# Performance work log

Hardware: AMD Instinct MI355X
Metric: run time of the kernel (lower is better)

Reference implementation:

```python
import jax, jax.numpy as jnp
import numpy as np

N, F_IN, F_HID, F_OUT, E = 100000, 128, 256, 40, 1600000
LOG_SQRT_2PI = 0.9189385332046727  # log(sqrt(2*pi))


def setup_inputs() -> dict:
    key = jax.random.key(0)
    ks = jax.random.split(key, 12)
    s_in = 1.0 / np.sqrt(F_IN)
    s_hid = 1.0 / np.sqrt(F_HID)
    s_out = 1.0 / np.sqrt(F_OUT)
    return {
        "x": jax.random.normal(ks[0], (N, F_IN), jnp.float32),
        "adj_row": jax.random.randint(ks[1], (E,), 0, N, jnp.int32),
        "adj_col": jax.random.randint(ks[2], (E,), 0, N, jnp.int32),
        "adj_val": jax.random.uniform(ks[3], (E,), jnp.float32) * 0.1,
        "eps": jax.random.normal(ks[4], (1, N, F_IN), jnp.float32),
        "Wz1": jax.random.normal(ks[5], (F_IN, F_IN), jnp.float32) * s_in,
        "bz1": jnp.zeros((F_IN,), jnp.float32),
        "Wz2": jax.random.normal(ks[6], (F_IN, 2 * F_IN), jnp.float32) * s_in,
        "bz2": jnp.zeros((2 * F_IN,), jnp.float32),
        "W0": jax.random.uniform(ks[7], (F_IN, F_HID), jnp.float32, -s_hid, s_hid),
        "b0": jax.random.uniform(ks[8], (F_HID,), jnp.float32, -s_hid, s_hid),
        "W1": jax.random.uniform(ks[9], (F_HID, F_OUT), jnp.float32, -s_out, s_out),
        "b1": jax.random.uniform(ks[10], (F_OUT,), jnp.float32, -s_out, s_out),
    }


def spmm(row, col, val, mat):
    # sparse [N,N] (COO) @ dense [N,D] -> [N,D] via gather + segment_sum
    return jax.ops.segment_sum(val[:, None] * mat[col], row, num_segments=mat.shape[0])


def reference(x, adj_row, adj_col, adj_val, eps, Wz1, bz1, Wz2, bz2, W0, b0, W1, b1):
    # z_w MLP: Linear -> ReLU -> Linear producing [N, 2*F_IN]
    feats = jax.nn.relu(x @ Wz1 + bz1) @ Wz2 + bz2
    z_x_hat = spmm(adj_row, adj_col, adj_val, feats)  # [N, 2*F_IN]
    mean = z_x_hat[:, :F_IN]
    std = jax.nn.softplus(z_x_hat[:, F_IN:]) + 0.01
    # rsample((1,)): [1, N, F_IN]
    z = mean[None] + std[None] * eps
    # diagonal Normal log-probs, summed over feature dim
    logq = (-0.5 * ((z - mean[None]) / std[None]) ** 2 - jnp.log(std)[None] - LOG_SQRT_2PI).sum(-1)
    logp = (-0.5 * z ** 2 - LOG_SQRT_2PI).sum(-1)
    l2 = (logq - logp).mean(0).mean()
    h = z.mean(0)  # [N, F_IN]
    # GCN layer 1: dense transform then spmm, relu (dropout off in eval)
    h = jax.nn.relu(spmm(adj_row, adj_col, adj_val, h @ W0) + b0)
    # GCN layer 2 (output)
    out = spmm(adj_row, adj_col, adj_val, h @ W1) + b1
    return jax.nn.log_softmax(out, axis=1), l2
```

## Files before the change

### kernel.cpp

```cpp
#include <hip/hip_runtime.h>
#include <math.h>

constexpr int NN = 100000;
constexpr int NCHUNK = 128;
constexpr int RROWS  = 12500;

using f32x4 = __attribute__((ext_vector_type(4))) float;
using s16x8 = __attribute__((ext_vector_type(8))) short;
using us8   = __attribute__((ext_vector_type(8))) unsigned short;
using us4   = __attribute__((ext_vector_type(4))) unsigned short;

__device__ __forceinline__ unsigned short f2bf(float f) {
    unsigned u = __float_as_uint(f);
    unsigned r = u + 0x7FFFu + ((u >> 16) & 1u);
    return (unsigned short)(r >> 16);
}
__device__ __forceinline__ float bf2f(unsigned short u) {
    return __uint_as_float(((unsigned)u) << 16);
}

__device__ __forceinline__ void wfrag_body(
    const float* __restrict__ W, short* __restrict__ Wf,
    int K, int NC, int tid)
{
    const int KK = K / 32;
    int lane = tid & 63, f = tid >> 6;
    int ncg = f / KK, kk = f % KK;
    int col = ncg * 16 + (lane & 15);
    int k0  = kk * 32 + 8 * (lane >> 4);
    s16x8 o;
    #pragma unroll
    for (int j = 0; j < 8; ++j)
        o[j] = (col < NC) ? (short)f2bf(W[(size_t)(k0 + j) * NC + col]) : (short)0;
    *reinterpret_cast<s16x8*>(Wf + (size_t)tid * 8) = o;
}

template<int K, int WM, int WN, int CB, int AK, bool OBF16, int BIASMODE, bool ORELU>
__device__ __forceinline__ void gemm_body(
    int bid, const void* __restrict__ Ain, const short* __restrict__ Wf,
    const float* __restrict__ bias, const float* __restrict__ b0,
    void* __restrict__ Cout, int M, int NCout)
{
    constexpr int KK = K / 32;
    const int tid = threadIdx.x;
    const int lane = tid & 63, wid = tid >> 6;
    const int wm = wid % WM, wn = wid / WM;
    const int rowBase = bid * (WM * 64) + wm * 64;
    const int cfb = wn * CB;
    const int l15 = lane & 15, lh = lane >> 4;

    f32x4 acc[4][CB];
    #pragma unroll
    for (int i = 0; i < 4; ++i)
        #pragma unroll
        for (int j = 0; j < CB; ++j) acc[i][j] = (f32x4)0.f;

    #pragma unroll
    for (int kk = 0; kk < KK; ++kk) {
        const int k0 = kk * 32 + lh * 8;
        s16x8 a[4];
        #pragma unroll
        for (int rb = 0; rb < 4; ++rb) {
            int row = rowBase + rb * 16 + l15;
            row = row < M ? row : M - 1;
            if (AK == 0) {
                const float* ap = (const float*)Ain + (size_t)row * K + k0;
                float4 u = *reinterpret_cast<const float4*>(ap);
                float4 v = *reinterpret_cast<const float4*>(ap + 4);
                a[rb][0] = (short)f2bf(u.x); a[rb][1] = (short)f2bf(u.y);
                a[rb][2] = (short)f2bf(u.z); a[rb][3] = (short)f2bf(u.w);
                a[rb][4] = (short)f2bf(v.x); a[rb][5] = (short)f2bf(v.y);
                a[rb][6] = (short)f2bf(v.z); a[rb][7] = (short)f2bf(v.w);
            } else if (AK == 1) {
                a[rb] = *reinterpret_cast<const s16x8*>((const short*)Ain + (size_t)row * K + k0);
            } else {
                s16x8 s = *reinterpret_cast<const s16x8*>((const short*)Ain + (size_t)row * K + k0);
                float4 ba = *reinterpret_cast<const float4*>(b0 + k0);
                float4 bb = *reinterpret_cast<const float4*>(b0 + k0 + 4);
                float bv[8] = {ba.x, ba.y, ba.z, ba.w, bb.x, bb.y, bb.z, bb.w};
                #pragma unroll
                for (int j = 0; j < 8; ++j) {
                    float fv = bf2f((unsigned short)s[j]) + bv[j];
                    a[rb][j] = (short)f2bf(fmaxf(fv, 0.f));
                }
            }
        }
        s16x8 b[CB];
        #pragma unroll
        for (int cb = 0; cb < CB; ++cb)
            b[cb] = *reinterpret_cast<const s16x8*>(
                Wf + ((size_t)((cfb + cb) * KK + kk) * 64 + lane) * 8);
        #pragma unroll
        for (int rb = 0; rb < 4; ++rb)
            #pragma unroll
            for (int cb = 0; cb < CB; ++cb)
                acc[rb][cb] = __builtin_amdgcn_mfma_f32_16x16x32_bf16(
                    a[rb], b[cb], acc[rb][cb], 0, 0, 0);
    }

    #pragma unroll
    for (int cb = 0; cb < CB; ++cb) {
        int col = (cfb + cb) * 16 + l15;
        if (col >= NCout) continue;
        float bs = (BIASMODE != 0) ? bias[col] : 0.f;
        #pragma unroll
        for (int rb = 0; rb < 4; ++rb) {
            #pragma unroll
            for (int r = 0; r < 4; ++r) {
                int row = rowBase + rb * 16 + lh * 4 + r;
                if (row >= M) continue;
                float v = acc[rb][cb][r];
                if (BIASMODE == 1) v += bs;
                if (ORELU) v = fmaxf(v, 0.f);
                if (OBF16)
                    ((unsigned short*)Cout)[(size_t)row * NCout + col] = f2bf(v);
                else
                    ((float*)Cout)[(size_t)row * NCout + col] = v;
            }
        }
    }
}

template<int K, int WM, int WN, int CB, int AK, bool OBF16, int BIASMODE, bool ORELU>
__global__ __launch_bounds__(WM * WN * 64) void gemm_mfma(
    const void* __restrict__ Ain, const short* __restrict__ Wf,
    const float* __restrict__ bias, const float* __restrict__ b0,
    void* __restrict__ Cout, int M, int NCout)
{
    gemm_body<K, WM, WN, CB, AK, OBF16, BIASMODE, ORELU>(
        blockIdx.x, Ain, Wf, bias, b0, Cout, M, NCout);
}

__device__ __forceinline__ void hist_body(
    const int* __restrict__ row, unsigned short* __restrict__ part,
    int E, int chunkE, int chunk, int rowLo, unsigned* lcnt)
{
    for (int i = threadIdx.x; i < RROWS / 4; i += 256) lcnt[i] = 0u;
    __syncthreads();
    const int e0 = chunk * chunkE;
    const int e1 = min(e0 + chunkE, E);
    for (int e = e0 + threadIdx.x; e < e1; e += 256) {
        int lr = row[e] - rowLo;
        if ((unsigned)lr < (unsigned)RROWS)
            atomicAdd(&lcnt[lr >> 2], 1u << ((lr & 3) << 3));
    }
    __syncthreads();
    unsigned* dst = reinterpret_cast<unsigned*>(part + (size_t)chunk * NN + rowLo);
    for (int i = threadIdx.x; i < RROWS / 4; i += 256) {
        unsigned w = lcnt[i];
        dst[2 * i + 0] = (w & 0xFFu) | (((w >> 8) & 0xFFu) << 16);
        dst[2 * i + 1] = ((w >> 16) & 0xFFu) | (((w >> 24) & 0xFFu) << 16);
    }
}

__device__ __forceinline__ void scatter_body(
    const int* __restrict__ row, const int* __restrict__ col,
    const float* __restrict__ val, const int* __restrict__ rp,
    const unsigned short* __restrict__ part, int2* __restrict__ edges,
    int E, int chunkE, int chunk, int rowLo, unsigned* lcnt)
{
    for (int i = threadIdx.x; i < RROWS / 4; i += 256) lcnt[i] = 0u;
    __syncthreads();
    const int e0 = chunk * chunkE;
    const int e1 = min(e0 + chunkE, E);
    const unsigned short* choff = part + (size_t)chunk * NN;
    for (int e = e0 + threadIdx.x; e < e1; e += 256) {
        int r = row[e];
        int lr = r - rowLo;
        if ((unsigned)lr < (unsigned)RROWS) {
            unsigned old = atomicAdd(&lcnt[lr >> 2], 1u << ((lr & 3) << 3));
            int local = (int)((old >> ((lr & 3) << 3)) & 0xFFu);
            int p = rp[r] + (int)choff[r] + local;
            edges[p] = make_int2(col[e], __float_as_int(val[e]));
        }
    }
}

__global__ __launch_bounds__(256) void hist_wfrag_combo(
    const int* __restrict__ arow, unsigned short* __restrict__ part,
    int E, int chunkE,
    const float* __restrict__ Wz1, const float* __restrict__ Wz2,
    const float* __restrict__ W0,  const float* __restrict__ W1,
    short* wz1f, short* wz2f, short* w0f, short* w1f)
{
    __shared__ unsigned lcnt[RROWS / 4];
    int b = blockIdx.x;
    if (b < NCHUNK * 8) {
        hist_body(arow, part, E, chunkE, b & (NCHUNK - 1), (b >> 7) * RROWS, lcnt);
    } else {
        int bb = b - NCHUNK * 8;
        if (bb < 8)       wfrag_body(Wz1, wz1f, 128, 128, bb * 256 + threadIdx.x);
        else if (bb < 24) wfrag_body(Wz2, wz2f, 128, 256, (bb - 8) * 256 + threadIdx.x);
        else if (bb < 40) wfrag_body(W0,  w0f,  128, 256, (bb - 24) * 256 + threadIdx.x);
        else {
            int tid = (bb - 40) * 256 + threadIdx.x;
            if (tid < 3 * 8 * 64) wfrag_body(W1, w1f, 256, 40, tid);
        }
    }
}

__global__ __launch_bounds__(256) void scatter_g1_combo(
    const int* __restrict__ arow, const int* __restrict__ acol,
    const float* __restrict__ aval, const int* __restrict__ rp,
    const unsigned short* __restrict__ part, int2* __restrict__ edges,
    int E, int chunkE,
    const float* __restrict__ x, const short* __restrict__ wz1f,
    const float* __restrict__ bz1, unsigned short* __restrict__ t1out)
{
    __shared__ unsigned lcnt[RROWS / 4];
    int b = blockIdx.x;
    if (b < NCHUNK * 8) {
        scatter_body(arow, acol, aval, rp, part, edges, E, chunkE,
                     b & (NCHUNK - 1), (b >> 7) * RROWS, lcnt);
    } else {
        gemm_body<128, 2, 2, 4, 0, true, 1, true>(
            b - NCHUNK * 8, x, wz1f, bz1, nullptr, t1out, NN, 128);
    }
}

__global__ __launch_bounds__(256) void chunk_scan(
    unsigned short* __restrict__ part, int* __restrict__ cnt)
{
    int r = blockIdx.x * 256 + threadIdx.x;
    if (r >= NN) return;
    int run = 0;
    for (int c0 = 0; c0 < NCHUNK; c0 += 8) {
        int v[8];
        #pragma unroll
        for (int j = 0; j < 8; ++j) v[j] = part[(size_t)(c0 + j) * NN + r];
        #pragma unroll
        for (int j = 0; j < 8; ++j) {
            part[(size_t)(c0 + j) * NN + r] = (unsigned short)run;
            run += v[j];
        }
    }
    cnt[r] = run;
}

__global__ __launch_bounds__(256) void scan_blk(
    const int* __restrict__ cnt, int* __restrict__ rp, int* __restrict__ bsums, int n)
{
    const int t = threadIdx.x;
    const int lane = t & 63, wid = t >> 6;
    const int base = blockIdx.x * 1024 + t * 4;
    int a0 = 0, a1 = 0, a2 = 0, a3 = 0;
    if (base + 3 < n) {
        int4 v = *reinterpret_cast<const int4*>(&cnt[base]);
        a0 = v.x; a1 = v.y; a2 = v.z; a3 = v.w;
    } else {
        if (base + 0 < n) a0 = cnt[base + 0];
        if (base + 1 < n) a1 = cnt[base + 1];
        if (base + 2 < n) a2 = cnt[base + 2];
        if (base + 3 < n) a3 = cnt[base + 3];
    }
    int s0 = a0, s1 = s0 + a1, s2 = s1 + a2, s3 = s2 + a3;
    int v = s3;
    #pragma unroll
    for (int o = 1; o < 64; o <<= 1) {
        int u = __shfl_up(v, o);
        if (lane >= o) v += u;
    }
    __shared__ int wtot[4];
    if (lane == 63) wtot[wid] = v;
    __syncthreads();
    int woff = 0;
    #pragma unroll
    for (int w = 0; w < 4; ++w) if (w < wid) woff += wtot[w];
    int texcl = woff + v - s3;
    if (base + 0 < n) rp[base + 0] = texcl;
    if (base + 1 < n) rp[base + 1] = texcl + s0;
    if (base + 2 < n) rp[base + 2] = texcl + s1;
    if (base + 3 < n) rp[base + 3] = texcl + s2;
    if (t == 255) bsums[blockIdx.x] = woff + v;
}

__global__ void scan_mid(const int* __restrict__ bsums, int* __restrict__ boff, int nb)
{
    if (threadIdx.x == 0 && blockIdx.x == 0) {
        int run = 0;
        for (int b = 0; b < nb; ++b) { boff[b] = run; run += bsums[b]; }
    }
}

__global__ __launch_bounds__(256) void scan_add(
    int* __restrict__ rp, const int* __restrict__ boff, int n, int E)
{
    int i = blockIdx.x * 256 + threadIdx.x;
    if (i < n) rp[i] += boff[i >> 10];
    if (i == 0) rp[n] = E;
}

template<bool RS>
__global__ __launch_bounds__(256) void spmm128(
    const int* __restrict__ rp, const int2* __restrict__ edges,
    const unsigned short* __restrict__ mat, unsigned short* __restrict__ out,
    float* __restrict__ rowsum)
{
    int gid = blockIdx.x * 256 + threadIdx.x;
    int r = gid >> 4, sl = gid & 15;
    if (r >= NN) return;
    const int beg = rp[r], end = rp[r + 1];
    float acc[8] = {};
    float vs = 0.f;
    int e = beg;
    for (; e + 7 < end; e += 8) {
        int2 c[8]; float v[8]; us8 f[8];
        #pragma unroll
        for (int k = 0; k < 8; ++k) c[k] = edges[e + k];
        #pragma unroll
        for (int k = 0; k < 8; ++k) {
            v[k] = __int_as_float(c[k].y);
            f[k] = *reinterpret_cast<const us8*>(mat + (size_t)c[k].x * 128 + sl * 8);
        }
        if (RS) vs += v[0] + v[1] + v[2] + v[3] + v[4] + v[5] + v[6] + v[7];
        #pragma unroll
        for (int k = 0; k < 8; ++k)
            #pragma unroll
            for (int j = 0; j < 8; ++j) acc[j] += v[k] * bf2f(f[k][j]);
    }
    for (; e + 3 < end; e += 4) {
        int2 c[4]; float v[4]; us8 f[4];
        #pragma unroll
        for (int k = 0; k < 4; ++k) c[k] = edges[e + k];
        #pragma unroll
        for (int k = 0; k < 4; ++k) {
            v[k] = __int_as_float(c[k].y);
            f[k] = *reinterpret_cast<const us8*>(mat + (size_t)c[k].x * 128 + sl * 8);
        }
        if (RS) vs += v[0] + v[1] + v[2] + v[3];
        #pragma unroll
        for (int k = 0; k < 4; ++k)
            #pragma unroll
            for (int j = 0; j < 8; ++j) acc[j] += v[k] * bf2f(f[k][j]);
    }
    for (; e < end; ++e) {
        int2 cv = edges[e];
        float v = __int_as_float(cv.y);
        if (RS) vs += v;
        us8 f = *reinterpret_cast<const us8*>(mat + (size_t)cv.x * 128 + sl * 8);
        #pragma unroll
        for (int j = 0; j < 8; ++j) acc[j] += v * bf2f(f[j]);
    }
    us8 o;
    #pragma unroll
    for (int j = 0; j < 8; ++j) o[j] = f2bf(acc[j]);
    *reinterpret_cast<us8*>(out + (size_t)r * 128 + sl * 8) = o;
    if (RS && sl == 0) rowsum[r] = vs;
}

__global__ __launch_bounds__(256) void gemm_z_sample(
    const unsigned short* __restrict__ A, const short* __restrict__ Wf,
    const float* __restrict__ bz2, const float* __restrict__ rowsum,
    const float* __restrict__ eps, unsigned short* __restrict__ hout,
    float* __restrict__ partials)
{
    const int tid = threadIdx.x;
    const int lane = tid & 63, wid = tid >> 6;
    const int rowBase = blockIdx.x * 64;
    const int l15 = lane & 15, lh = lane >> 4;

    const int cf[4] = {wid * 2, wid * 2 + 1, 8 + wid * 2, 8 + wid * 2 + 1};

    f32x4 acc[4][4];
    #pragma unroll
    for (int i = 0; i < 4; ++i)
        #pragma unroll
        for (int j = 0; j < 4; ++j) acc[i][j] = (f32x4)0.f;

    #pragma unroll
    for (int kk = 0; kk < 4; ++kk) {
        const int k0 = kk * 32 + lh * 8;
        s16x8 a[4];
        #pragma unroll
        for (int rb = 0; rb < 4; ++rb) {
            int row = rowBase + rb * 16 + l15;
            row = row < NN ? row : NN - 1;
            a[rb] = *reinterpret_cast<const s16x8*>(A + (size_t)row * 128 + k0);
        }
        s16x8 b[4];
        #pragma unroll
        for (int cb = 0; cb < 4; ++cb)
            b[cb] = *reinterpret_cast<const s16x8*>(
                Wf + ((size_t)(cf[cb] * 4 + kk) * 64 + lane) * 8);
        #pragma unroll
        for (int rb = 0; rb < 4; ++rb)
            #pragma unroll
            for (int cb = 0; cb < 4; ++cb)
                acc[rb][cb] = __builtin_amdgcn_mfma_f32_16x16x32_bf16(
                    a[rb], b[cb], acc[rb][cb], 0, 0, 0);
    }

    const float bsm0 = bz2[wid * 32 + l15];
    const float bsm1 = bz2[wid * 32 + 16 + l15];
    const float bss0 = bz2[128 + wid * 32 + l15];
    const float bss1 = bz2[128 + wid * 32 + 16 + l15];
    float p = 0.f;
    #pragma unroll
    for (int rb = 0; rb < 4; ++rb) {
        #pragma unroll
        for (int r = 0; r < 4; ++r) {
            int row = rowBase + rb * 16 + lh * 4 + r;
            if (row >= NN) continue;
            float rs = rowsum[row];
            #pragma unroll
            for (int cb = 0; cb < 2; ++cb) {
                int colm = wid * 32 + cb * 16 + l15;
                float mean = acc[rb][cb][r]     + rs * (cb ? bsm1 : bsm0);
                float sv   = acc[rb][2 + cb][r] + rs * (cb ? bss1 : bss0);
                float ea = __expf(-fabsf(sv));
                float sp = fmaxf(sv, 0.f) + __logf(1.f + ea);
                float sd = sp + 0.01f;
                float e  = eps[(size_t)row * 128 + colm];
                float h  = mean + sd * e;
                hout[(size_t)row * 128 + colm] = f2bf(h);
                p += 0.5f * h * h - 0.5f * e * e - __logf(sd);
            }
        }
    }
    #pragma unroll
    for (int o = 32; o > 0; o >>= 1) p += __shfl_xor(p, o);
    __shared__ float ws[4];
    if (lane == 0) ws[wid] = p;
    __syncthreads();
    if (tid == 0) partials[blockIdx.x] = ws[0] + ws[1] + ws[2] + ws[3];
}

__global__ __launch_bounds__(256) void spmm40_lsm(
    const int* __restrict__ rp, const int2* __restrict__ edges,
    const unsigned short* __restrict__ mat, const float* __restrict__ b1,
    float* __restrict__ out)
{
    int gid = blockIdx.x * 256 + threadIdx.x;
    int r = gid >> 4, sl = gid & 15;
    const int beg = rp[r], end = rp[r + 1];
    float4 acc = make_float4(0.f, 0.f, 0.f, 0.f);
    int e = beg;
    for (; e + 3 < end; e += 4) {
        int2 c[4];
        #pragma unroll
        for (int k = 0; k < 4; ++k) c[k] = edges[e + k];
        if (sl < 10) {
            #pragma unroll
            for (int k = 0; k < 4; ++k) {
                float v = __int_as_float(c[k].y);
                us4 m = *reinterpret_cast<const us4*>(mat + (size_t)c[k].x * 40 + sl * 4);
                acc.x += v * bf2f(m[0]); acc.y += v * bf2f(m[1]);
                acc.z += v * bf2f(m[2]); acc.w += v * bf2f(m[3]);
            }
        }
    }
    for (; e < end; ++e) {
        int2 cv = edges[e];
        float v = __int_as_float(cv.y);
        if (sl < 10) {
            us4 m = *reinterpret_cast<const us4*>(mat + (size_t)cv.x * 40 + sl * 4);
            acc.x += v * bf2f(m[0]); acc.y += v * bf2f(m[1]);
            acc.z += v * bf2f(m[2]); acc.w += v * bf2f(m[3]);
        }
    }
    float xv[4] = {-1e30f, -1e30f, -1e30f, -1e30f};
    if (sl < 10) {
        xv[0] = acc.x + b1[sl * 4 + 0]; xv[1] = acc.y + b1[sl * 4 + 1];
        xv[2] = acc.z + b1[sl * 4 + 2]; xv[3] = acc.w + b1[sl * 4 + 3];
    }
    float m = fmaxf(fmaxf(xv[0], xv[1]), fmaxf(xv[2], xv[3]));
    #pragma unroll
    for (int o = 1; o < 16; o <<= 1) m = fmaxf(m, __shfl_xor(m, o, 16));
    float ssum = 0.f;
    #pragma unroll
    for (int k = 0; k < 4; ++k) ssum += (sl < 10) ? __expf(xv[k] - m) : 0.f;
    #pragma unroll
    for (int o = 1; o < 16; o <<= 1) ssum += __shfl_xor(ssum, o, 16);
    if (sl < 10) {
        float lse = m + __logf(ssum);
        float4 o4 = make_float4(xv[0] - lse, xv[1] - lse, xv[2] - lse, xv[3] - lse);
        *reinterpret_cast<float4*>(out + (size_t)r * 40 + sl * 4) = o4;
    }
}

__global__ __launch_bounds__(256) void finalize_l2(
    const float* __restrict__ partials, int np, float* __restrict__ out)
{
    double a = 0.0;
    for (int i = threadIdx.x; i < np; i += 256) a += (double)partials[i];
    #pragma unroll
    for (int o = 32; o > 0; o >>= 1) a += __shfl_xor(a, o);
    __shared__ double ws[4];
    if ((threadIdx.x & 63) == 0) ws[threadIdx.x >> 6] = a;
    __syncthreads();
    if (threadIdx.x == 0)
        out[(size_t)NN * 40] = (float)((ws[0] + ws[1] + ws[2] + ws[3]) / (double)NN);
}

extern "C" void kernel_launch(void* const* d_in, const int* in_sizes, int n_in,
                              void* d_out, int out_size, void* d_ws, size_t ws_size,
                              hipStream_t stream)
{
    const float* x    = (const float*)d_in[0];
    const int*   arow = (const int*)d_in[1];
    const int*   acol = (const int*)d_in[2];
    const float* aval = (const float*)d_in[3];
    const float* eps  = (const float*)d_in[4];
    const float* Wz1  = (const float*)d_in[5];
    const float* bz1  = (const float*)d_in[6];
    const float* Wz2  = (const float*)d_in[7];
    const float* bz2  = (const float*)d_in[8];
    const float* W0   = (const float*)d_in[9];
    const float* b0   = (const float*)d_in[10];
    const float* W1   = (const float*)d_in[11];
    const float* b1   = (const float*)d_in[12];
    float* out = (float*)d_out;
    const int E = in_sizes[1];

    char* p = (char*)d_ws;
    auto alloc = [&](size_t bytes) {
        char* q = p;
        p += (bytes + 15) & ~(size_t)15;
        return (void*)q;
    };
    int2* edges           = (int2*)alloc((size_t)E * 8);
    unsigned short* part  = (unsigned short*)alloc((size_t)NCHUNK * NN * 2);
    int*  rp              = (int*)alloc((size_t)(NN + 4) * 4);
    int*  cnt             = (int*)alloc((size_t)NN * 4);
    float* rowsum         = (float*)alloc((size_t)NN * 4);
    int*  bsums           = (int*)alloc(128 * 4);
    int*  boff            = (int*)alloc(128 * 4);
    float* partials       = (float*)alloc(1568 * 4);
    unsigned short* bufT  = (unsigned short*)alloc((size_t)NN * 128 * 2);
    unsigned short* bufU  = (unsigned short*)alloc((size_t)NN * 128 * 2);
    unsigned short* bufZ  = (unsigned short*)alloc((size_t)NN * 256 * 2);
    short* wz1f           = (short*)alloc(8  * 4 * 64 * 8 * 2);
    short* wz2f           = (short*)alloc(16 * 4 * 64 * 8 * 2);
    short* w0f            = (short*)alloc(16 * 4 * 64 * 8 * 2);
    short* w1f            = (short*)alloc(3  * 8 * 64 * 8 * 2);

    dim3 blk(256);
    const int nScan = (NN + 1023) / 1024;
    const int gSp = (NN * 16) / 256;
    const int gZ  = (NN + 63) / 64;
    const int chunkE = (E + NCHUNK - 1) / NCHUNK;
    const int gHist = NCHUNK * 8;

    hist_wfrag_combo<<<dim3(gHist + 46), blk, 0, stream>>>(
        arow, part, E, chunkE, Wz1, Wz2, W0, W1, wz1f, wz2f, w0f, w1f);
    chunk_scan<<<dim3((NN + 255) / 256), blk, 0, stream>>>(part, cnt);
    scan_blk<<<dim3(nScan), blk, 0, stream>>>(cnt, rp, bsums, NN);
    scan_mid<<<dim3(1), dim3(64), 0, stream>>>(bsums, boff, nScan);
    scan_add<<<dim3((NN + 256) / 256), blk, 0, stream>>>(rp, boff, NN, E);
    scatter_g1_combo<<<dim3(gHist + 782), blk, 0, stream>>>(
        arow, acol, aval, rp, part, edges, E, chunkE, x, wz1f, bz1, bufT);
    spmm128<true><<<dim3(gSp), blk, 0, stream>>>(rp, edges, bufT, bufU, rowsum);
    gemm_z_sample<<<dim3(gZ), blk, 0, stream>>>(bufU, wz2f, bz2, rowsum, eps, bufU, partials);
    spmm128<false><<<dim3(gSp), blk, 0, stream>>>(rp, edges, bufU, bufT, nullptr);
    gemm_mfma<128, 1, 4, 4, 1, true, 0, false><<<dim3(gZ), blk, 0, stream>>>(
        bufT, w0f, nullptr, nullptr, bufZ, NN, 256);
    gemm_mfma<256, 4, 1, 3, 2, true, 0, false><<<dim3(391), blk, 0, stream>>>(
        bufZ, w1f, nullptr, b0, bufT, NN, 40);
    spmm40_lsm<<<dim3(gSp), blk, 0, stream>>>(rp, edges, bufT, b1, out);
    finalize_l2<<<dim3(1), blk, 0, stream>>>(partials, gZ, out);
}
```

Baseline: 438.9 us.

## Sort edges by column within rows and pad final layer output to 64 columns

Adds a per-row insertion sort of CSR edges by column index, meant to improve gather locality in the three SpMM passes. It also pads the second GCN layer's output to a 64-column stride: the weight fragments gain a fourth column tile and the GEMM writes 64 columns. The final SpMM then lets all 16 lanes load aligned 8-byte chunks without the sl<10 branch. The cost is an extra sort kernel with poor parallelism (one thread per row, using LDS), more gathered bytes per row in the last SpMM, and extra padded GEMM work. Rows with more than 48 edges are left unsorted.

Result: slower. 519.7 us (+18.4%).

```diff
diff --git a/kernel.cpp b/kernel.cpp
--- a/kernel.cpp
+++ b/kernel.cpp
@@ -192,10 +192,7 @@
         if (bb < 8)       wfrag_body(Wz1, wz1f, 128, 128, bb * 256 + threadIdx.x);
         else if (bb < 24) wfrag_body(Wz2, wz2f, 128, 256, (bb - 8) * 256 + threadIdx.x);
         else if (bb < 40) wfrag_body(W0,  w0f,  128, 256, (bb - 24) * 256 + threadIdx.x);
-        else {
-            int tid = (bb - 40) * 256 + threadIdx.x;
-            if (tid < 3 * 8 * 64) wfrag_body(W1, w1f, 256, 40, tid);
-        }
+        else              wfrag_body(W1,  w1f,  256, 40, (bb - 40) * 256 + threadIdx.x);
     }
 }
 
@@ -216,6 +213,26 @@
         gemm_body<128, 2, 2, 4, 0, true, 1, true>(
             b - NCHUNK * 8, x, wz1f, bz1, nullptr, t1out, NN, 128);
     }
+}
+
+__global__ __launch_bounds__(64) void rowsort_k(
+    const int* __restrict__ rp, int2* __restrict__ edges)
+{
+    __shared__ int2 buf[64][49];
+    int r = blockIdx.x * 64 + threadIdx.x;
+    if (r >= NN) return;
+    const int beg = rp[r];
+    const int d = rp[r + 1] - beg;
+    if (d <= 1 || d > 48) return;
+    int2* b = buf[threadIdx.x];
+    for (int i = 0; i < d; ++i) b[i] = edges[beg + i];
+    for (int i = 1; i < d; ++i) {
+        int2 key = b[i];
+        int j = i - 1;
+        while (j >= 0 && b[j].x > key.x) { b[j + 1] = b[j]; --j; }
+        b[j + 1] = key;
+    }
+    for (int i = 0; i < d; ++i) edges[beg + i] = b[i];
 }
 
 __global__ __launch_bounds__(256) void chunk_scan(
@@ -439,36 +456,34 @@
         int2 c[4];
         #pragma unroll
         for (int k = 0; k < 4; ++k) c[k] = edges[e + k];
-        if (sl < 10) {
-            #pragma unroll
-            for (int k = 0; k < 4; ++k) {
-                float v = __int_as_float(c[k].y);
-                us4 m = *reinterpret_cast<const us4*>(mat + (size_t)c[k].x * 40 + sl * 4);
-                acc.x += v * bf2f(m[0]); acc.y += v * bf2f(m[1]);
-                acc.z += v * bf2f(m[2]); acc.w += v * bf2f(m[3]);
-            }
+        #pragma unroll
+        for (int k = 0; k < 4; ++k) {
+            float v = __int_as_float(c[k].y);
+            us4 m = *reinterpret_cast<const us4*>(mat + (size_t)c[k].x * 64 + sl * 4);
+            acc.x += v * bf2f(m[0]); acc.y += v * bf2f(m[1]);
+            acc.z += v * bf2f(m[2]); acc.w += v * bf2f(m[3]);
         }
     }
     for (; e < end; ++e) {
         int2 cv = edges[e];
         float v = __int_as_float(cv.y);
-        if (sl < 10) {
-            us4 m = *reinterpret_cast<const us4*>(mat + (size_t)cv.x * 40 + sl * 4);
-            acc.x += v * bf2f(m[0]); acc.y += v * bf2f(m[1]);
-            acc.z += v * bf2f(m[2]); acc.w += v * bf2f(m[3]);
-        }
-    }
-    float xv[4] = {-1e30f, -1e30f, -1e30f, -1e30f};
-    if (sl < 10) {
-        xv[0] = acc.x + b1[sl * 4 + 0]; xv[1] = acc.y + b1[sl * 4 + 1];
-        xv[2] = acc.z + b1[sl * 4 + 2]; xv[3] = acc.w + b1[sl * 4 + 3];
+        us4 m = *reinterpret_cast<const us4*>(mat + (size_t)cv.x * 64 + sl * 4);
+        acc.x += v * bf2f(m[0]); acc.y += v * bf2f(m[1]);
+        acc.z += v * bf2f(m[2]); acc.w += v * bf2f(m[3]);
+    }
+    float av[4] = {acc.x, acc.y, acc.z, acc.w};
+    float xv[4];
+    #pragma unroll
+    for (int k = 0; k < 4; ++k) {
+        int col = sl * 4 + k;
+        xv[k] = (col < 40) ? av[k] + b1[col] : -1e30f;
     }
     float m = fmaxf(fmaxf(xv[0], xv[1]), fmaxf(xv[2], xv[3]));
     #pragma unroll
     for (int o = 1; o < 16; o <<= 1) m = fmaxf(m, __shfl_xor(m, o, 16));
     float ssum = 0.f;
     #pragma unroll
-    for (int k = 0; k < 4; ++k) ssum += (sl < 10) ? __expf(xv[k] - m) : 0.f;
+    for (int k = 0; k < 4; ++k) ssum += (sl * 4 + k < 40) ? __expf(xv[k] - m) : 0.f;
     #pragma unroll
     for (int o = 1; o < 16; o <<= 1) ssum += __shfl_xor(ssum, o, 16);
     if (sl < 10) {
@@ -532,7 +547,7 @@
     short* wz1f           = (short*)alloc(8  * 4 * 64 * 8 * 2);
     short* wz2f           = (short*)alloc(16 * 4 * 64 * 8 * 2);
     short* w0f            = (short*)alloc(16 * 4 * 64 * 8 * 2);
-    short* w1f            = (short*)alloc(3  * 8 * 64 * 8 * 2);
+    short* w1f            = (short*)alloc(4  * 8 * 64 * 8 * 2);
 
     dim3 blk(256);
     const int nScan = (NN + 1023) / 1024;
@@ -541,7 +556,7 @@
     const int chunkE = (E + NCHUNK - 1) / NCHUNK;
     const int gHist = NCHUNK * 8;
 
-    hist_wfrag_combo<<<dim3(gHist + 46), blk, 0, stream>>>(
+    hist_wfrag_combo<<<dim3(gHist + 48), blk, 0, stream>>>(
         arow, part, E, chunkE, Wz1, Wz2, W0, W1, wz1f, wz2f, w0f, w1f);
     chunk_scan<<<dim3((NN + 255) / 256), blk, 0, stream>>>(part, cnt);
     scan_blk<<<dim3(nScan), blk, 0, stream>>>(cnt, rp, bsums, NN);
@@ -549,13 +564,14 @@
     scan_add<<<dim3((NN + 256) / 256), blk, 0, stream>>>(rp, boff, NN, E);
     scatter_g1_combo<<<dim3(gHist + 782), blk, 0, stream>>>(
         arow, acol, aval, rp, part, edges, E, chunkE, x, wz1f, bz1, bufT);
+    rowsort_k<<<dim3((NN + 63) / 64), dim3(64), 0, stream>>>(rp, edges);
     spmm128<true><<<dim3(gSp), blk, 0, stream>>>(rp, edges, bufT, bufU, rowsum);
     gemm_z_sample<<<dim3(gZ), blk, 0, stream>>>(bufU, wz2f, bz2, rowsum, eps, bufU, partials);
     spmm128<false><<<dim3(gSp), blk, 0, stream>>>(rp, edges, bufU, bufT, nullptr);
     gemm_mfma<128, 1, 4, 4, 1, true, 0, false><<<dim3(gZ), blk, 0, stream>>>(
         bufT, w0f, nullptr, nullptr, bufZ, NN, 256);
-    gemm_mfma<256, 4, 1, 3, 2, true, 0, false><<<dim3(391), blk, 0, stream>>>(
-        bufZ, w1f, nullptr, b0, bufT, NN, 40);
+    gemm_mfma<256, 4, 1, 4, 2, true, 0, false><<<dim3(391), blk, 0, stream>>>(
+        bufZ, w1f, nullptr, b0, bufT, NN, 64);
     spmm40_lsm<<<dim3(gSp), blk, 0, stream>>>(rp, edges, bufT, b1, out);
     finalize_l2<<<dim3(1), blk, 0, stream>>>(partials, gZ, out);
 }
```
